# Performance work log

Measured on AMD Instinct MI355X. Metric: run time of the kernel, lower is better.

## Reference

```python
import jax, jax.numpy as jnp
import numpy as np

# DeepSeek-V3-style gate config
TOP_K = 8
N_EXPERTS = 256
N_GROUP = 8
TOPK_GROUP = 4
ROUTED_SCALING = 2.5
EPS = 1e-20


def setup_inputs() -> dict:
    key = jax.random.key(0)
    k1, k2, k3 = jax.random.split(key, 3)
    S, H = 16384, 7168
    hidden_states = jax.random.normal(k1, (S, H), dtype=jnp.float32)
    weight = jax.random.normal(k2, (N_EXPERTS, H), dtype=jnp.float32) * 0.02
    e_score_correction_bias = jax.random.normal(k3, (N_EXPERTS,), dtype=jnp.float32) * 0.1
    return {"hidden_states": hidden_states, "weight": weight,
            "e_score_correction_bias": e_score_correction_bias}


def reference(hidden_states, weight, e_score_correction_bias):
    S = hidden_states.shape[0]
    group_size = N_EXPERTS // N_GROUP  # 32

    # gating GEMM: [S, E]
    router_logits = jnp.einsum('sh,eh->se', hidden_states, weight)
    # scoring_func == 'sigmoid'
    scores = jax.nn.sigmoid(router_logits)
    scores_for_choice = scores + e_score_correction_bias[None, :]

    # group scores: sum of top-2 biased scores within each group -> [S, G]
    grouped = scores_for_choice.reshape(S, N_GROUP, group_size)
    top2_vals, _ = jax.lax.top_k(grouped, 2)
    group_scores = top2_vals.sum(axis=-1)

    # select top `TOPK_GROUP` groups, build group mask
    _, group_idx = jax.lax.top_k(group_scores, TOPK_GROUP)  # [S, topk_group]
    group_mask = jnp.zeros((S, N_GROUP), dtype=scores.dtype)
    group_mask = group_mask.at[jnp.arange(S)[:, None], group_idx].set(1.0)
    score_mask = jnp.repeat(group_mask, group_size, axis=-1)  # [S, E]

    # masked top-k over experts; weights gathered from UNBIASED scores
    tmp_scores = jnp.where(score_mask > 0, scores_for_choice, 0.0)
    _, topk_idx = jax.lax.top_k(tmp_scores, TOP_K)  # [S, top_k]
    topk_weight = jnp.take_along_axis(scores, topk_idx, axis=1)

    # renormalize (top_k > 1 and norm_topk_prob) then scale (noaux_tc)
    denom = topk_weight.sum(axis=-1, keepdims=True) + EPS
    topk_weight = topk_weight / denom * ROUTED_SCALING
    return topk_weight, topk_idx
```

## Files before the change

### kernel.cpp

```cpp
#include <hip/hip_runtime.h>
#include <math.h>

#define H_DIM 7168
#define N_EXP 256
#define N_GRP 8
#define G_SZ  32
#define TOPK_G 4
#define TOPK   8
#define BM 64
#define BK 32
#define S_TOK 16384
#define NTILES (H_DIM / BK)
#define NSPLIT 2
#define NH     (NTILES / NSPLIT)
#define ITILES 4
#define NINT   (NH / ITILES)
#define TILE_W_BYTES 32768

#define SA_SCALE 256.0f
#define SW_SCALE 4096.0f
#define DESCALE  (1.0f / 1048576.0f)

__device__ __align__(256) char g_wimg[(size_t)NTILES * TILE_W_BYTES];
__device__ __align__(256) float g_part[NSPLIT * (size_t)S_TOK * N_EXP];

typedef __attribute__((ext_vector_type(8))) _Float16 f16x8;
typedef __attribute__((ext_vector_type(4))) float f32x4;
typedef __attribute__((ext_vector_type(4))) unsigned short u16x4;
typedef __attribute__((ext_vector_type(8))) unsigned short u16x8;

__device__ inline void split2h(float x, unsigned short& h, unsigned short& l) {
    _Float16 hf = (_Float16)x;
    _Float16 lf = (_Float16)(x - (float)hf);
    h = __builtin_bit_cast(unsigned short, hf);
    l = __builtin_bit_cast(unsigned short, lf);
}

__global__ __launch_bounds__(256)
void convert_w_kernel(const float* __restrict__ W) {
    int idx  = blockIdx.x * 256 + threadIdx.x;
    int e    = idx / (H_DIM / 8);
    int koct = idx - e * (H_DIM / 8);
    int k0   = koct * 8;
    int t    = k0 >> 5;
    int o    = (k0 >> 3) & 3;
    int lane = (e & 15) | (o << 4);
    int w    = e >> 5;
    int nj   = (e >> 4) & 1;
    const float* src = W + (size_t)e * H_DIM + k0;
    unsigned short h[8], l[8];
    #pragma unroll
    for (int j = 0; j < 8; ++j)
        split2h(src[j] * SW_SCALE, h[j], l[j]);
    char* base = g_wimg + (size_t)t * TILE_W_BYTES + (w << 12) + (lane << 4);
    *(u16x8*)(base + nj * 1024)       = u16x8{h[0],h[1],h[2],h[3],h[4],h[5],h[6],h[7]};
    *(u16x8*)(base + (2 + nj) * 1024) = u16x8{l[0],l[1],l[2],l[3],l[4],l[5],l[6],l[7]};
}

__global__ __launch_bounds__(512, 4)
void moe_gemm_half(const float* __restrict__ A)
{
    __shared__ __align__(128) char smem[2 * ITILES * 8192];

    const int tid   = threadIdx.x;
    const int lane  = tid & 63;
    const int wave  = tid >> 6;
    const int khalf = blockIdx.x & 1;
    const int brow  = (blockIdx.x >> 1) * BM;
    const int g0    = khalf * NH;

    const int fr   = lane & 15;
    const int fkb  = (lane >> 4) << 4;
    const int fswz = ((fr << 6) + fkb) ^ ((fr & 7) << 4);

    const int ar   = tid >> 3;
    const int akq  = tid & 7;
    const int aswz = ((ar << 6) + (akq << 3)) ^ ((ar & 7) << 4);
    const float4* Ag4 = reinterpret_cast<const float4*>(
        A + (size_t)(brow + ar) * H_DIM + khalf * (H_DIM / NSPLIT)) + akq;

    const char* wsrc = g_wimg + (size_t)g0 * TILE_W_BYTES + (wave << 12) + (lane << 4);

    f32x4 acc[4][2] = {};

    auto loadW = [&](int t, f16x8& h0, f16x8& h1, f16x8& l0, f16x8& l1) {
        const char* p = wsrc + (size_t)t * TILE_W_BYTES;
        h0 = *(const f16x8*)(p + 0);
        h1 = *(const f16x8*)(p + 1024);
        l0 = *(const f16x8*)(p + 2048);
        l1 = *(const f16x8*)(p + 3072);
    };

    auto writeA = [&](const float4& v, char* ab) {
        unsigned short h[4], l[4];
        split2h(v.x * SA_SCALE, h[0], l[0]); split2h(v.y * SA_SCALE, h[1], l[1]);
        split2h(v.z * SA_SCALE, h[2], l[2]); split2h(v.w * SA_SCALE, h[3], l[3]);
        *(u16x4*)(ab + aswz)        = u16x4{h[0], h[1], h[2], h[3]};
        *(u16x4*)(ab + 4096 + aswz) = u16x4{l[0], l[1], l[2], l[3]};
    };

    auto compute = [&](const char* ab, f16x8 bh0, f16x8 bh1, f16x8 bl0, f16x8 bl1) {
        f16x8 ah[4], al[4];
        #pragma unroll
        for (int mi = 0; mi < 4; ++mi) {
            ah[mi] = *(const f16x8*)(ab + mi * 1024 + fswz);
            al[mi] = *(const f16x8*)(ab + 4096 + mi * 1024 + fswz);
        }
        #pragma unroll
        for (int mi = 0; mi < 4; ++mi)
            acc[mi][0] = __builtin_amdgcn_mfma_f32_16x16x32_f16(ah[mi], bh0, acc[mi][0], 0, 0, 0);
        #pragma unroll
        for (int mi = 0; mi < 4; ++mi)
            acc[mi][1] = __builtin_amdgcn_mfma_f32_16x16x32_f16(ah[mi], bh1, acc[mi][1], 0, 0, 0);
        #pragma unroll
        for (int mi = 0; mi < 4; ++mi)
            acc[mi][0] = __builtin_amdgcn_mfma_f32_16x16x32_f16(al[mi], bh0, acc[mi][0], 0, 0, 0);
        #pragma unroll
        for (int mi = 0; mi < 4; ++mi)
            acc[mi][1] = __builtin_amdgcn_mfma_f32_16x16x32_f16(al[mi], bh1, acc[mi][1], 0, 0, 0);
        #pragma unroll
        for (int mi = 0; mi < 4; ++mi)
            acc[mi][0] = __builtin_amdgcn_mfma_f32_16x16x32_f16(ah[mi], bl0, acc[mi][0], 0, 0, 0);
        #pragma unroll
        for (int mi = 0; mi < 4; ++mi)
            acc[mi][1] = __builtin_amdgcn_mfma_f32_16x16x32_f16(ah[mi], bl1, acc[mi][1], 0, 0, 0);
    };

    f16x8 xh0, xh1, xl0, xl1;
    f16x8 yh0, yh1, yl0, yl1;

    {
        char* b0 = smem;
        float4 a0[ITILES];
        #pragma unroll
        for (int s = 0; s < ITILES; ++s) a0[s] = Ag4[(size_t)s * 8];
        loadW(0, xh0, xh1, xl0, xl1);
        loadW(1, yh0, yh1, yl0, yl1);
        #pragma unroll
        for (int s = 0; s < ITILES; ++s) writeA(a0[s], b0 + s * 8192);
        asm volatile("s_waitcnt lgkmcnt(0)" ::: "memory");
        __builtin_amdgcn_s_barrier();
    }

    #pragma unroll 1
    for (int i = 0; i < NINT; ++i) {
        char* cur = smem + (i & 1) * (ITILES * 8192);
        char* nxt = smem + ((i + 1) & 1) * (ITILES * 8192);
        const bool havenext = (i + 1 < NINT);
        const int ibase = (havenext ? i + 1 : i) * ITILES;

        float4 an[ITILES];
        #pragma unroll
        for (int s = 0; s < ITILES; ++s) an[s] = Ag4[(size_t)(ibase + s) * 8];

        #pragma unroll
        for (int s = 0; s < ITILES; ++s) {
            const int t = i * ITILES + s;
            const int tpf = (t + 2 < NH) ? t + 2 : NH - 1;
            f16x8 nh0, nh1, nl0, nl1;
            loadW(tpf, nh0, nh1, nl0, nl1);
            compute(cur + s * 8192, xh0, xh1, xl0, xl1);
            if (s == 1 && havenext) {
                #pragma unroll
                for (int ss = 0; ss < ITILES; ++ss)
                    writeA(an[ss], nxt + ss * 8192);
            }
            xh0 = yh0; xh1 = yh1; xl0 = yl0; xl1 = yl1;
            yh0 = nh0; yh1 = nh1; yl0 = nl0; yl1 = nl1;
        }
        asm volatile("s_waitcnt lgkmcnt(0)" ::: "memory");
        __builtin_amdgcn_s_barrier();
    }

    float* pb = g_part + ((size_t)khalf * S_TOK + brow) * N_EXP;
    #pragma unroll
    for (int mi = 0; mi < 4; ++mi)
        #pragma unroll
        for (int nj = 0; nj < 2; ++nj)
            #pragma unroll
            for (int q = 0; q < 4; ++q) {
                int row = mi * 16 + ((lane >> 4) << 2) + q;
                int col = wave * 32 + nj * 16 + (lane & 15);
                pb[row * N_EXP + col] = acc[mi][nj][q];
            }
}

__global__ __launch_bounds__(256)
void gate_kernel(const float* __restrict__ bias, float* __restrict__ out, int S)
{
    const int lane = threadIdx.x & 63;
    const int row  = (blockIdx.x * 256 + threadIdx.x) >> 6;

    const float4 p0 = *(const float4*)(g_part + (size_t)row * N_EXP + lane * 4);
    const float4 p1 = *(const float4*)(g_part + ((size_t)S_TOK + row) * N_EXP + lane * 4);
    const float4 b4 = *(const float4*)(bias + lane * 4);

    float s[4], v[4];
    float m1 = -1e30f, m2 = -1e30f;
    {
        const float* q0 = (const float*)&p0;
        const float* q1 = (const float*)&p1;
        const float* qb = (const float*)&b4;
        #pragma unroll
        for (int j = 0; j < 4; ++j) {
            float x = (q0[j] + q1[j]) * DESCALE;
            s[j] = 1.0f / (1.0f + expf(-x));
            float sb = s[j] + qb[j];
            v[j] = sb;
            if (sb > m1) { m2 = m1; m1 = sb; } else if (sb > m2) { m2 = sb; }
        }
    }
    #pragma unroll
    for (int d = 1; d < 8; d <<= 1) {
        float om1 = __shfl_xor(m1, d), om2 = __shfl_xor(m2, d);
        float hi = fmaxf(m1, om1), lo = fminf(m1, om1);
        m1 = hi;
        m2 = fmaxf(lo, fmaxf(m2, om2));
    }
    float gs = m1 + m2;
    float gsv[8];
    #pragma unroll
    for (int g = 0; g < 8; ++g) gsv[g] = __shfl(gs, g << 3);

    unsigned gmask = 0;
    #pragma unroll
    for (int t = 0; t < TOPK_G; ++t) {
        float best = -1e30f; int bg = 0;
        #pragma unroll
        for (int g = 0; g < 8; ++g) {
            bool avail = !((gmask >> g) & 1);
            if (avail && gsv[g] > best) { best = gsv[g]; bg = g; }
        }
        gmask |= 1u << bg;
    }

    const bool sel = (gmask >> (lane >> 3)) & 1;
    #pragma unroll
    for (int j = 0; j < 4; ++j) v[j] = sel ? v[j] : 0.0f;

    float wv[TOPK]; int wi[TOPK]; float wsum = 0.0f;
    #pragma unroll
    for (int t = 0; t < TOPK; ++t) {
        float bv = v[0]; int bj = 0;
        #pragma unroll
        for (int j = 1; j < 4; ++j)
            if (v[j] > bv) { bv = v[j]; bj = j; }
        int bidx = (lane << 2) | bj;
        #pragma unroll
        for (int d = 32; d >= 1; d >>= 1) {
            float ov = __shfl_xor(bv, d);
            int   oi = __shfl_xor(bidx, d);
            if (ov > bv || (ov == bv && oi < bidx)) { bv = ov; bidx = oi; }
        }
        int ol = bidx >> 2, oj = bidx & 3;
        float sl = s[0];
        if (oj == 1) sl = s[1]; else if (oj == 2) sl = s[2]; else if (oj == 3) sl = s[3];
        float sv = __shfl(sl, ol);
        wv[t] = sv; wi[t] = bidx; wsum += sv;
        if (lane == ol) {
            if (oj == 0) v[0] = -1e30f; else if (oj == 1) v[1] = -1e30f;
            else if (oj == 2) v[2] = -1e30f; else v[3] = -1e30f;
        }
    }

    if (lane == 0) {
        float scale = 2.5f / (wsum + 1e-20f);
        #pragma unroll
        for (int t = 0; t < TOPK; ++t) {
            out[(size_t)row * TOPK + t] = wv[t] * scale;
            out[(size_t)S * TOPK + (size_t)row * TOPK + t] = (float)wi[t];
        }
    }
}

extern "C" void kernel_launch(void* const* d_in, const int* in_sizes, int n_in,
                              void* d_out, int out_size, void* d_ws, size_t ws_size,
                              hipStream_t stream) {
    const float* A    = (const float*)d_in[0];
    const float* W    = (const float*)d_in[1];
    const float* bias = (const float*)d_in[2];
    float* out = (float*)d_out;
    const int S = in_sizes[0] / H_DIM;

    convert_w_kernel<<<dim3(N_EXP * (H_DIM / 8) / 256), 256, 0, stream>>>(W);
    moe_gemm_half<<<dim3(NSPLIT * S / BM), 512, 0, stream>>>(A);
    gate_kernel<<<dim3(S / 4), 256, 0, stream>>>(bias, out, S);
}
```

Baseline: 218.7 us.

## Restructure GEMM main loop into two-tile ping-pong with register-prefetched LDS fragments

Replaces the four-tile-per-stage LDS pipeline with a two-tile stage whose A fragments are loaded from LDS into double-buffered registers ahead of the MFMA passes. Weight loads for the next tile are issued between the split-precision MFMA passes, and each pass is wrapped in s_setprio to favour matrix issue. The goal is to hide LDS and global load latency behind MFMA work and to halve LDS usage, which may help occupancy. The cost is one barrier per two tiles instead of per four, plus higher register pressure from the buffered fragments.

```diff
diff --git a/kernel.cpp b/kernel.cpp
--- a/kernel.cpp
+++ b/kernel.cpp
@@ -13,8 +13,7 @@
 #define NTILES (H_DIM / BK)
 #define NSPLIT 2
 #define NH     (NTILES / NSPLIT)
-#define ITILES 4
-#define NINT   (NH / ITILES)
+#define NINT   (NH / 2)
 #define TILE_W_BYTES 32768
 
 #define SA_SCALE 256.0f
@@ -60,14 +59,13 @@
 __global__ __launch_bounds__(512, 4)
 void moe_gemm_half(const float* __restrict__ A)
 {
-    __shared__ __align__(128) char smem[2 * ITILES * 8192];
+    __shared__ __align__(128) char smem[2 * 16384];
 
     const int tid   = threadIdx.x;
     const int lane  = tid & 63;
     const int wave  = tid >> 6;
     const int khalf = blockIdx.x & 1;
     const int brow  = (blockIdx.x >> 1) * BM;
-    const int g0    = khalf * NH;
 
     const int fr   = lane & 15;
     const int fkb  = (lane >> 4) << 4;
@@ -79,18 +77,61 @@
     const float4* Ag4 = reinterpret_cast<const float4*>(
         A + (size_t)(brow + ar) * H_DIM + khalf * (H_DIM / NSPLIT)) + akq;
 
-    const char* wsrc = g_wimg + (size_t)g0 * TILE_W_BYTES + (wave << 12) + (lane << 4);
+    const char* wsrc = g_wimg + (size_t)(khalf * NH) * TILE_W_BYTES
+                       + (wave << 12) + (lane << 4);
 
     f32x4 acc[4][2] = {};
 
-    auto loadW = [&](int t, f16x8& h0, f16x8& h1, f16x8& l0, f16x8& l1) {
-        const char* p = wsrc + (size_t)t * TILE_W_BYTES;
-        h0 = *(const f16x8*)(p + 0);
-        h1 = *(const f16x8*)(p + 1024);
-        l0 = *(const f16x8*)(p + 2048);
-        l1 = *(const f16x8*)(p + 3072);
-    };
-
+    f16x8 WH0[2], WH1[2], WL0[2], WL1[2];
+    f16x8 AH[2][4], AL[2][4];
+
+    auto issueW = [&](int t, int p) {
+        const char* b = wsrc + (size_t)t * TILE_W_BYTES;
+        WH0[p] = *(const f16x8*)(b + 0);
+        WH1[p] = *(const f16x8*)(b + 1024);
+        WL0[p] = *(const f16x8*)(b + 2048);
+        WL1[p] = *(const f16x8*)(b + 3072);
+    };
+    auto issueAH = [&](const char* sb, int p) {
+        #pragma unroll
+        for (int mi = 0; mi < 4; ++mi)
+            AH[p][mi] = *(const f16x8*)(sb + mi * 1024 + fswz);
+    };
+    auto issueAL = [&](const char* sb, int p) {
+        #pragma unroll
+        for (int mi = 0; mi < 4; ++mi)
+            AL[p][mi] = *(const f16x8*)(sb + 4096 + mi * 1024 + fswz);
+    };
+    auto passHH = [&](int p) {
+        __builtin_amdgcn_s_setprio(1);
+        #pragma unroll
+        for (int mi = 0; mi < 4; ++mi)
+            acc[mi][0] = __builtin_amdgcn_mfma_f32_16x16x32_f16(AH[p][mi], WH0[p], acc[mi][0], 0, 0, 0);
+        #pragma unroll
+        for (int mi = 0; mi < 4; ++mi)
+            acc[mi][1] = __builtin_amdgcn_mfma_f32_16x16x32_f16(AH[p][mi], WH1[p], acc[mi][1], 0, 0, 0);
+        __builtin_amdgcn_s_setprio(0);
+    };
+    auto passLH = [&](int p) {
+        __builtin_amdgcn_s_setprio(1);
+        #pragma unroll
+        for (int mi = 0; mi < 4; ++mi)
+            acc[mi][0] = __builtin_amdgcn_mfma_f32_16x16x32_f16(AL[p][mi], WH0[p], acc[mi][0], 0, 0, 0);
+        #pragma unroll
+        for (int mi = 0; mi < 4; ++mi)
+            acc[mi][1] = __builtin_amdgcn_mfma_f32_16x16x32_f16(AL[p][mi], WH1[p], acc[mi][1], 0, 0, 0);
+        __builtin_amdgcn_s_setprio(0);
+    };
+    auto passHL = [&](int p) {
+        __builtin_amdgcn_s_setprio(1);
+        #pragma unroll
+        for (int mi = 0; mi < 4; ++mi)
+            acc[mi][0] = __builtin_amdgcn_mfma_f32_16x16x32_f16(AH[p][mi], WL0[p], acc[mi][0], 0, 0, 0);
+        #pragma unroll
+        for (int mi = 0; mi < 4; ++mi)
+            acc[mi][1] = __builtin_amdgcn_mfma_f32_16x16x32_f16(AH[p][mi], WL1[p], acc[mi][1], 0, 0, 0);
+        __builtin_amdgcn_s_setprio(0);
+    };
     auto writeA = [&](const float4& v, char* ab) {
         unsigned short h[4], l[4];
         split2h(v.x * SA_SCALE, h[0], l[0]); split2h(v.y * SA_SCALE, h[1], l[1]);
@@ -99,77 +140,47 @@
         *(u16x4*)(ab + 4096 + aswz) = u16x4{l[0], l[1], l[2], l[3]};
     };
 
-    auto compute = [&](const char* ab, f16x8 bh0, f16x8 bh1, f16x8 bl0, f16x8 bl1) {
-        f16x8 ah[4], al[4];
-        #pragma unroll
-        for (int mi = 0; mi < 4; ++mi) {
-            ah[mi] = *(const f16x8*)(ab + mi * 1024 + fswz);
-            al[mi] = *(const f16x8*)(ab + 4096 + mi * 1024 + fswz);
-        }
-        #pragma unroll
-        for (int mi = 0; mi < 4; ++mi)
-            acc[mi][0] = __builtin_amdgcn_mfma_f32_16x16x32_f16(ah[mi], bh0, acc[mi][0], 0, 0, 0);
-        #pragma unroll
-        for (int mi = 0; mi < 4; ++mi)
-            acc[mi][1] = __builtin_amdgcn_mfma_f32_16x16x32_f16(ah[mi], bh1, acc[mi][1], 0, 0, 0);
-        #pragma unroll
-        for (int mi = 0; mi < 4; ++mi)
-            acc[mi][0] = __builtin_amdgcn_mfma_f32_16x16x32_f16(al[mi], bh0, acc[mi][0], 0, 0, 0);
-        #pragma unroll
-        for (int mi = 0; mi < 4; ++mi)
-            acc[mi][1] = __builtin_amdgcn_mfma_f32_16x16x32_f16(al[mi], bh1, acc[mi][1], 0, 0, 0);
-        #pragma unroll
-        for (int mi = 0; mi < 4; ++mi)
-            acc[mi][0] = __builtin_amdgcn_mfma_f32_16x16x32_f16(ah[mi], bl0, acc[mi][0], 0, 0, 0);
-        #pragma unroll
-        for (int mi = 0; mi < 4; ++mi)
-            acc[mi][1] = __builtin_amdgcn_mfma_f32_16x16x32_f16(ah[mi], bl1, acc[mi][1], 0, 0, 0);
-    };
-
-    f16x8 xh0, xh1, xl0, xl1;
-    f16x8 yh0, yh1, yl0, yl1;
-
     {
-        char* b0 = smem;
-        float4 a0[ITILES];
-        #pragma unroll
-        for (int s = 0; s < ITILES; ++s) a0[s] = Ag4[(size_t)s * 8];
-        loadW(0, xh0, xh1, xl0, xl1);
-        loadW(1, yh0, yh1, yl0, yl1);
-        #pragma unroll
-        for (int s = 0; s < ITILES; ++s) writeA(a0[s], b0 + s * 8192);
+        float4 a0 = Ag4[0], a1 = Ag4[8];
+        issueW(0, 0);
+        writeA(a0, smem);
+        writeA(a1, smem + 8192);
         asm volatile("s_waitcnt lgkmcnt(0)" ::: "memory");
         __builtin_amdgcn_s_barrier();
+        issueAH(smem, 0);
+        issueAL(smem, 0);
     }
 
     #pragma unroll 1
     for (int i = 0; i < NINT; ++i) {
-        char* cur = smem + (i & 1) * (ITILES * 8192);
-        char* nxt = smem + ((i + 1) & 1) * (ITILES * 8192);
-        const bool havenext = (i + 1 < NINT);
-        const int ibase = (havenext ? i + 1 : i) * ITILES;
-
-        float4 an[ITILES];
-        #pragma unroll
-        for (int s = 0; s < ITILES; ++s) an[s] = Ag4[(size_t)(ibase + s) * 8];
-
-        #pragma unroll
-        for (int s = 0; s < ITILES; ++s) {
-            const int t = i * ITILES + s;
-            const int tpf = (t + 2 < NH) ? t + 2 : NH - 1;
-            f16x8 nh0, nh1, nl0, nl1;
-            loadW(tpf, nh0, nh1, nl0, nl1);
-            compute(cur + s * 8192, xh0, xh1, xl0, xl1);
-            if (s == 1 && havenext) {
-                #pragma unroll
-                for (int ss = 0; ss < ITILES; ++ss)
-                    writeA(an[ss], nxt + ss * 8192);
-            }
-            xh0 = yh0; xh1 = yh1; xl0 = yl0; xl1 = yl1;
-            yh0 = nh0; yh1 = nh1; yl0 = nl0; yl1 = nl1;
-        }
+        char* cur = smem + (i & 1) * 16384;
+        char* nxt = smem + ((i + 1) & 1) * 16384;
+        const int t0 = i * 2;
+        const bool hn = (i + 1 < NINT);
+
+        float4 an0, an1;
+        if (hn) { an0 = Ag4[(size_t)(t0 + 2) * 8]; an1 = Ag4[(size_t)(t0 + 3) * 8]; }
+        issueW(t0 + 1, 1);
+        issueAH(cur + 8192, 1);
+        passHH(0);
+        passLH(0);
+        issueAL(cur + 8192, 1);
+        passHL(0);
+
+        if (hn) {
+            issueW(t0 + 2, 0);
+            writeA(an0, nxt);
+            writeA(an1, nxt + 8192);
+        }
+        passHH(1);
+        passLH(1);
+        passHL(1);
         asm volatile("s_waitcnt lgkmcnt(0)" ::: "memory");
         __builtin_amdgcn_s_barrier();
+        if (hn) {
+            issueAH(nxt, 0);
+            issueAL(nxt, 0);
+        }
     }
 
     float* pb = g_part + ((size_t)khalf * S_TOK + brow) * N_EXP;
```

After: 472.4 us. +116.0%, slower.
